# Kernel tuning notes

Hardware: AMD Instinct MI355X
Metric: run time of the kernel (lower is better)

Reference implementation:

```python
import jax, jax.numpy as jnp
import numpy as np

N_SAMPLES = 2048
BURN_IN = 128
STEP_SIZE = 0.1
D = 512   # walker dimension
H = 1024  # wavefunction MLP hidden width


def setup_inputs() -> dict:
    key = jax.random.key(0)
    k0, k1, k2 = jax.random.split(key, 3)
    x0 = jax.random.normal(k0, (1, D), dtype=jnp.float32)
    W1 = jax.random.normal(k1, (D, H), dtype=jnp.float32) / np.float32(np.sqrt(D))
    b1 = jnp.zeros((H,), dtype=jnp.float32)
    W2 = jax.random.normal(k2, (H, 1), dtype=jnp.float32) / np.float32(np.sqrt(H))
    b2 = jnp.zeros((1,), dtype=jnp.float32)
    return {"x0": x0, "W1": W1, "b1": b1, "W2": W2, "b2": b2}


def _model(x, W1, b1, W2, b2):
    # wavefunction MLP: [1, D] -> [1, 1]
    return jnp.tanh(x @ W1 + b1) @ W2 + b2


def reference(x0, W1, b1, W2, b2):
    def psi2(x):
        # model(x).pow(2)[0] -> shape [1]
        return (_model(x, W1, b1, W2, b2) ** 2)[0]

    def mh_step(x, k):
        k_noise, k_unif = jax.random.split(k)
        x_new = x + jax.random.normal(k_noise, x.shape, dtype=x.dtype) * STEP_SIZE
        p_new = psi2(x_new)
        p_old = psi2(x)
        ratio = jnp.minimum(p_new / (p_old + 1e-12), 1.0)          # clamp(max=1.0)
        u = jax.random.uniform(k_unif, ratio.shape, dtype=x.dtype)
        accept = (u < ratio).astype(x.dtype)[:, None]               # [1, 1]
        x = accept * x_new + (1.0 - accept) * x
        return x, x[0]  # carry chain state, record sample row [D]

    keys = jax.random.split(jax.random.key(1), N_SAMPLES + BURN_IN)
    _, traj = jax.lax.scan(mh_step, x0, keys)   # traj: [N+BURN_IN, D]
    return traj[BURN_IN:]                        # [N_SAMPLES, D]
```

## Files before the change

kernel.cpp:

```cpp
#include <hip/hip_runtime.h>
#include <stdint.h>
#include <math.h>


#define T_TOTAL 2176
#define NITER   1088
#define NROWS   2177
#define NBURN   128
#define DDIM    512
#define HDIM    1024
#define DONE_FLAG 0x13572468u

__device__ __forceinline__ uint2 tf2x32(uint32_t k0, uint32_t k1,
                                        uint32_t x0, uint32_t x1) {
  uint32_t ks2 = k0 ^ k1 ^ 0x1BD11BDAu;
  x0 += k0; x1 += k1;
#define TF_R(r) { x0 += x1; x1 = (x1 << (r)) | (x1 >> (32 - (r))); x1 ^= x0; }
  TF_R(13) TF_R(15) TF_R(26) TF_R(6)
  x0 += k1;  x1 += ks2 + 1u;
  TF_R(17) TF_R(29) TF_R(16) TF_R(24)
  x0 += ks2; x1 += k0 + 2u;
  TF_R(13) TF_R(15) TF_R(26) TF_R(6)
  x0 += k0;  x1 += k1 + 3u;
  TF_R(17) TF_R(29) TF_R(16) TF_R(24)
  x0 += k1;  x1 += ks2 + 4u;
  TF_R(13) TF_R(15) TF_R(26) TF_R(6)
  x0 += ks2; x1 += k0 + 5u;
#undef TF_R
  return make_uint2(x0, x1);
}

__device__ __forceinline__ float erfinv_xla(float x) {
  float w = -log1pf(-x * x);
  float p;
  if (w < 5.0f) {
    w = w - 2.5f;
    p = 2.81022636e-08f;
    p = fmaf(p, w, 3.43273939e-07f);
    p = fmaf(p, w, -3.5233877e-06f);
    p = fmaf(p, w, -4.39150654e-06f);
    p = fmaf(p, w, 0.00021858087f);
    p = fmaf(p, w, -0.00125372503f);
    p = fmaf(p, w, -0.00417768164f);
    p = fmaf(p, w, 0.246640727f);
    p = fmaf(p, w, 1.50140941f);
  } else {
    w = sqrtf(w) - 3.0f;
    p = -0.000200214257f;
    p = fmaf(p, w, 0.000100950558f);
    p = fmaf(p, w, 0.00134934322f);
    p = fmaf(p, w, -0.00367342844f);
    p = fmaf(p, w, 0.00573950773f);
    p = fmaf(p, w, -0.0076224613f);
    p = fmaf(p, w, 0.00943887047f);
    p = fmaf(p, w, 1.00167406f);
    p = fmaf(p, w, 2.83297682f);
  }
  return p * x;
}

__device__ __forceinline__ float normal_from_bits(uint32_t bits) {
  const float lo = -0.99999994f;
  float u01 = __uint_as_float(0x3f800000u | (bits >> 9)) - 1.0f;
  float v = u01 * 2.0f + lo;
  v = fmaxf(lo, v);
  return 1.41421356237309515f * erfinv_xla(v);
}

__device__ __forceinline__ float tanh_fast(float x) {
  float a = x * 2.88539008177792681472f;
#if __has_builtin(__builtin_amdgcn_exp2f)
  float e = __builtin_amdgcn_exp2f(a);
#else
  float e = exp2f(a);
#endif
  float r = __builtin_amdgcn_rcpf(e + 1.0f);
  return fmaf(-2.0f, r, 1.0f);
}

__global__ void __launch_bounds__(256) rng_kernel(const float* __restrict__ x0,
                                                  float* __restrict__ A,
                                                  float* __restrict__ U) {
  const uint32_t t = blockIdx.x;
  const int tid = threadIdx.x;
  uint2 kt = tf2x32(0u, 1u, 0u, t);
  uint2 kn = tf2x32(kt.x, kt.y, 0u, 0u);
  uint2 e0 = tf2x32(kn.x, kn.y, 0u, (uint32_t)tid);
  uint2 e1 = tf2x32(kn.x, kn.y, 0u, (uint32_t)(tid + 256));
  float n0 = normal_from_bits(e0.x ^ e0.y);
  float n1 = normal_from_bits(e1.x ^ e1.y);
  float* Arow = A + (size_t)(t + 1) * DDIM;
  Arow[tid]       = n0 * 0.1f;
  Arow[tid + 256] = n1 * 0.1f;
  if (tid == 0) {
    uint2 ku = tf2x32(kt.x, kt.y, 0u, 1u);
    uint2 eu = tf2x32(ku.x, ku.y, 0u, 0u);
    U[t] = __uint_as_float(0x3f800000u | ((eu.x ^ eu.y) >> 9)) - 1.0f;
  }
  if (t == 0) {
    A[tid]       = x0[tid];
    A[tid + 256] = x0[tid + 256];
  }
}

__global__ void __launch_bounds__(512) gemm_kernel(const float* __restrict__ A,
                                                   const float* __restrict__ W1,
                                                   float* __restrict__ Z,
                                                   int nrows) {
  const int r0 = blockIdx.x * 8;
  const int t  = threadIdx.x;
  const int c0 = t, c1 = t + 512;
  double acc[8][2];
#pragma unroll
  for (int r = 0; r < 8; ++r) { acc[r][0] = 0.0; acc[r][1] = 0.0; }
  for (int d = 0; d < 512; d += 4) {
    double wA[4], wB[4];
#pragma unroll
    for (int j = 0; j < 4; ++j) {
      wA[j] = (double)W1[(size_t)(d + j) * 1024 + c0];
      wB[j] = (double)W1[(size_t)(d + j) * 1024 + c1];
    }
#pragma unroll
    for (int r = 0; r < 8; ++r) {
      int rr = r0 + r; if (rr >= nrows) rr = nrows - 1;
      const float4 a4 = *(const float4*)(A + (size_t)rr * 512 + d);
      double a0 = (double)a4.x, a1 = (double)a4.y;
      double a2 = (double)a4.z, a3 = (double)a4.w;
      acc[r][0] += (a0 * wA[0] + a1 * wA[1]) + (a2 * wA[2] + a3 * wA[3]);
      acc[r][1] += (a0 * wB[0] + a1 * wB[1]) + (a2 * wB[2] + a3 * wB[3]);
    }
  }
  const int rmax = (nrows - r0 < 8) ? (nrows - r0) : 8;
  for (int r = 0; r < rmax; ++r) {
    Z[(size_t)(r0 + r) * 1024 + c0] = (float)acc[r][0];
    Z[(size_t)(r0 + r) * 1024 + c1] = (float)acc[r][1];
  }
}

#define DPP_ADD(v, ctrl)                                                     \
  v += __int_as_float(__builtin_amdgcn_update_dpp(                           \
      0, __float_as_int(v), (ctrl), 0xF, 0xF, true))

__device__ __forceinline__ float wave_reduce_to_last(float v) {
  DPP_ADD(v, 0xB1);
  DPP_ADD(v, 0x4E);
  DPP_ADD(v, 0x141);
  DPP_ADD(v, 0x140);
  DPP_ADD(v, 0x142);
  DPP_ADD(v, 0x143);
  return v;
}

#define BAR() asm volatile("s_waitcnt lgkmcnt(0)\n\ts_barrier" ::: "memory")

__global__ void __launch_bounds__(256) chain_kernel(
    const float* __restrict__ Z, const float* __restrict__ A,
    const float* __restrict__ U, const float* __restrict__ x0,
    const float* __restrict__ b1, const float* __restrict__ W2,
    const float* __restrict__ b2, float* __restrict__ out,
    unsigned* __restrict__ flag) {
  const int tid = threadIdx.x;

  if (blockIdx.x != 0) {
    float acc = (float)tid * 1.0e-6f;
    for (int i = 0; i < 4000; ++i) {
#pragma unroll
      for (int jj = 0; jj < 256; ++jj) acc = fmaf(acc, 0.99999988f, 1.0e-7f);
      unsigned f = __hip_atomic_load(flag, __ATOMIC_RELAXED,
                                     __HIP_MEMORY_SCOPE_AGENT);
      if (f == DONE_FLAG) break;
    }
    if (acc == 123456.75f && tid == 1023) out[0] = acc;
    return;
  }

  const int lane = tid & 63;
  const int wid = tid >> 6;
  __shared__ __align__(16) float wsum[2][3][4];
  __shared__ float Uld[2184];

  const float4* Zv = (const float4*)Z;
  const float2* Av = (const float2*)A;

  for (int i = tid; i < 2184; i += 256) Uld[i] = U[i];

  const float4 w2v = ((const float4*)W2)[tid];
  const float4 b1v = ((const float4*)b1)[tid];
  const float b2v = b2[0];

  float4 z0r = Zv[tid];
  float4 z1r = Zv[256 + tid];
  float4 z2r = Zv[512 + tid];
  float4 zA0 = Zv[3 * 256 + tid], zB0 = Zv[4 * 256 + tid];
  float4 zA1 = Zv[5 * 256 + tid], zB1 = Zv[6 * 256 + tid];
  float2 dAa0 = Av[1 * 256 + tid], dAb0 = Av[2 * 256 + tid];
  float2 dAa1 = Av[3 * 256 + tid], dAb1 = Av[4 * 256 + tid];

  double Y0 = (double)z0r.x + (double)b1v.x;
  double Y1 = (double)z0r.y + (double)b1v.y;
  double Y2 = (double)z0r.z + (double)b1v.z;
  double Y3 = (double)z0r.w + (double)b1v.w;

  float xa = x0[2 * tid], xb = x0[2 * tid + 1];

  __syncthreads();

  {
    float g0 = tanh_fast((float)Y0);
    float g1 = tanh_fast((float)Y1);
    float g2 = tanh_fast((float)Y2);
    float g3 = tanh_fast((float)Y3);
    float tm = fmaf(g3, w2v.w, fmaf(g2, w2v.z, fmaf(g1, w2v.y, g0 * w2v.x)));
    tm = wave_reduce_to_last(tm);
    if (lane == 63) wsum[1][0][wid] = tm;
  }
  __syncthreads();
  float p;
  {
    const float4 pp = *(const float4*)wsum[1][0];
    float m0 = ((pp.x + pp.y) + (pp.z + pp.w)) + b2v;
    p = m0 * m0;
  }
  float um1 = Uld[0] * (p + 1e-12f);
  float u2c = Uld[1];

  double Ya0 = Y0 + (double)z1r.x, Ya1 = Y1 + (double)z1r.y;
  double Ya2 = Y2 + (double)z1r.z, Ya3 = Y3 + (double)z1r.w;
  double Yb0 = Y0 + (double)z2r.x, Yb1 = Y1 + (double)z2r.y;
  double Yb2 = Y2 + (double)z2r.z, Yb3 = Y3 + (double)z2r.w;
  double Yc0 = Ya0 + (double)z2r.x, Yc1 = Ya1 + (double)z2r.y;
  double Yc2 = Ya2 + (double)z2r.z, Yc3 = Ya3 + (double)z2r.w;
  {
    float a0 = tanh_fast((float)Ya0), a1 = tanh_fast((float)Ya1);
    float a2 = tanh_fast((float)Ya2), a3 = tanh_fast((float)Ya3);
    float b0 = tanh_fast((float)Yb0), b1_ = tanh_fast((float)Yb1);
    float b2_ = tanh_fast((float)Yb2), b3 = tanh_fast((float)Yb3);
    float c0 = tanh_fast((float)Yc0), c1 = tanh_fast((float)Yc1);
    float c2 = tanh_fast((float)Yc2), c3 = tanh_fast((float)Yc3);
    float tA = fmaf(a3, w2v.w, fmaf(a2, w2v.z, fmaf(a1, w2v.y, a0 * w2v.x)));
    float tB = fmaf(b3, w2v.w, fmaf(b2_, w2v.z, fmaf(b1_, w2v.y, b0 * w2v.x)));
    float tC = fmaf(c3, w2v.w, fmaf(c2, w2v.z, fmaf(c1, w2v.y, c0 * w2v.x)));
    tA = wave_reduce_to_last(tA);
    tB = wave_reduce_to_last(tB);
    tC = wave_reduce_to_last(tC);
    if (lane == 63) {
      wsum[0][0][wid] = tA;
      wsum[0][1][wid] = tB;
      wsum[0][2][wid] = tC;
    }
  }
  __syncthreads();

#define ITER(k, PAR, ZAB, ZBB, DAB, DBB)                                     \
  {                                                                          \
    float u1n = Uld[2 * (k) + 2];                                            \
    float u2n = Uld[2 * (k) + 3];                                            \
    const float4 e1 = *(const float4*)wsum[PAR][0];                          \
    const float4 e2 = *(const float4*)wsum[PAR][1];                          \
    const float4 e3 = *(const float4*)wsum[PAR][2];                          \
    float m1 = ((e1.x + e1.y) + (e1.z + e1.w)) + b2v;                        \
    float q1 = m1 * m1;                                                      \
    bool a1v = um1 < q1;                                                     \
    float p1 = a1v ? q1 : p;                                                 \
    float um2 = u2c * (p1 + 1e-12f);                                         \
    float m2v = ((e2.x + e2.y) + (e2.z + e2.w)) + b2v;                       \
    float m3v = ((e3.x + e3.y) + (e3.z + e3.w)) + b2v;                       \
    float m23 = a1v ? m3v : m2v;                                             \
    float q23 = m23 * m23;                                                   \
    bool a2v = um2 < q23;                                                    \
    p = a2v ? q23 : p1;                                                      \
    float xat = a1v ? xa + DAB.x : xa;                                       \
    float xbt = a1v ? xb + DAB.y : xb;                                       \
    xa = a2v ? xat + DBB.x : xat;                                            \
    xb = a2v ? xbt + DBB.y : xbt;                                            \
    if ((k) >= 64) {                                                         \
      float2 o1; o1.x = xat; o1.y = xbt;                                     \
      *(float2*)(out + (size_t)(2 * (k) - NBURN) * DDIM + 2 * tid) = o1;     \
      float2 o2; o2.x = xa; o2.y = xb;                                       \
      *(float2*)(out + (size_t)(2 * (k) + 1 - NBURN) * DDIM + 2 * tid) = o2; \
    }                                                                        \
    DAB = Av[(size_t)(2 * (k) + 5) * 256 + tid];                             \
    DBB = Av[(size_t)(2 * (k) + 6) * 256 + tid];                             \
            \
    Y0 = a1v ? (a2v ? Yc0 : Ya0) : (a2v ? Yb0 : Y0);                         \
    Y1 = a1v ? (a2v ? Yc1 : Ya1) : (a2v ? Yb1 : Y1);                         \
    Y2 = a1v ? (a2v ? Yc2 : Ya2) : (a2v ? Yb2 : Y2);                         \
    Y3 = a1v ? (a2v ? Yc3 : Ya3) : (a2v ? Yb3 : Y3);                         \
                         \
    Ya0 = Y0 + (double)ZAB.x;  Ya1 = Y1 + (double)ZAB.y;                     \
    Ya2 = Y2 + (double)ZAB.z;  Ya3 = Y3 + (double)ZAB.w;                     \
    Yb0 = Y0 + (double)ZBB.x;  Yb1 = Y1 + (double)ZBB.y;                     \
    Yb2 = Y2 + (double)ZBB.z;  Yb3 = Y3 + (double)ZBB.w;                     \
    Yc0 = Ya0 + (double)ZBB.x; Yc1 = Ya1 + (double)ZBB.y;                    \
    Yc2 = Ya2 + (double)ZBB.z; Yc3 = Ya3 + (double)ZBB.w;                    \
    ZAB = Zv[(size_t)(2 * (k) + 7) * 256 + tid];                             \
    ZBB = Zv[(size_t)(2 * (k) + 8) * 256 + tid];                             \
    float ga0 = tanh_fast((float)Ya0), ga1 = tanh_fast((float)Ya1);          \
    float ga2 = tanh_fast((float)Ya2), ga3 = tanh_fast((float)Ya3);          \
    float gb0 = tanh_fast((float)Yb0), gb1 = tanh_fast((float)Yb1);          \
    float gb2 = tanh_fast((float)Yb2), gb3 = tanh_fast((float)Yb3);          \
    float gc0 = tanh_fast((float)Yc0), gc1 = tanh_fast((float)Yc1);          \
    float gc2 = tanh_fast((float)Yc2), gc3 = tanh_fast((float)Yc3);          \
    float tA = fmaf(ga3, w2v.w, fmaf(ga2, w2v.z, fmaf(ga1, w2v.y, ga0 * w2v.x))); \
    float tB = fmaf(gb3, w2v.w, fmaf(gb2, w2v.z, fmaf(gb1, w2v.y, gb0 * w2v.x))); \
    float tC = fmaf(gc3, w2v.w, fmaf(gc2, w2v.z, fmaf(gc1, w2v.y, gc0 * w2v.x))); \
    tA = wave_reduce_to_last(tA);                                            \
    tB = wave_reduce_to_last(tB);                                            \
    tC = wave_reduce_to_last(tC);                                            \
    if (lane == 63) {                                                        \
      wsum[(PAR) ^ 1][0][wid] = tA;                                          \
      wsum[(PAR) ^ 1][1][wid] = tB;                                          \
      wsum[(PAR) ^ 1][2][wid] = tC;                                          \
    }                                                                        \
    um1 = u1n * (p + 1e-12f);                                                \
    u2c = u2n;                                                               \
    BAR();                                                                   \
  }

  for (int k = 0; k < NITER; k += 2) {
    ITER(k,     0, zA0, zB0, dAa0, dAb0);
    ITER(k + 1, 1, zA1, zB1, dAa1, dAb1);
  }
#undef ITER

  if (tid == 0) {
    __hip_atomic_store(flag, DONE_FLAG, __ATOMIC_RELAXED,
                       __HIP_MEMORY_SCOPE_AGENT);
  }
}

extern "C" void kernel_launch(void* const* d_in, const int* in_sizes, int n_in,
                              void* d_out, int out_size, void* d_ws, size_t ws_size,
                              hipStream_t stream) {
  const float* x0 = (const float*)d_in[0];
  const float* W1 = (const float*)d_in[1];
  const float* b1 = (const float*)d_in[2];
  const float* W2 = (const float*)d_in[3];
  const float* b2 = (const float*)d_in[4];
  float* out = (float*)d_out;

  char* ws = (char*)d_ws;
  float* A = (float*)ws;
  float* Z = (float*)(ws + 4472832);
  float* U = (float*)(ws + 4472832 + 8945664);
  unsigned* flag = (unsigned*)(ws + 4472832 + 8945664 + 8736);

  rng_kernel<<<T_TOTAL, 256, 0, stream>>>(x0, A, U);
  gemm_kernel<<<273, 512, 0, stream>>>(A, W1, Z, NROWS);
  chain_kernel<<<256, 256, 0, stream>>>(Z, A, U, x0, b1, W2, b2, out, flag);
}
```

Before: 861.8 us.

## Widen chain kernel to 512 threads and double GEMM rows per block

```diff
diff --git a/kernel.cpp b/kernel.cpp
--- a/kernel.cpp
+++ b/kernel.cpp
@@ -107,12 +107,12 @@
                                                    const float* __restrict__ W1,
                                                    float* __restrict__ Z,
                                                    int nrows) {
-  const int r0 = blockIdx.x * 8;
+  const int r0 = blockIdx.x * 16;
   const int t  = threadIdx.x;
   const int c0 = t, c1 = t + 512;
-  double acc[8][2];
+  double acc[16][2];
 #pragma unroll
-  for (int r = 0; r < 8; ++r) { acc[r][0] = 0.0; acc[r][1] = 0.0; }
+  for (int r = 0; r < 16; ++r) { acc[r][0] = 0.0; acc[r][1] = 0.0; }
   for (int d = 0; d < 512; d += 4) {
     double wA[4], wB[4];
 #pragma unroll
@@ -121,7 +121,7 @@
       wB[j] = (double)W1[(size_t)(d + j) * 1024 + c1];
     }
 #pragma unroll
-    for (int r = 0; r < 8; ++r) {
+    for (int r = 0; r < 16; ++r) {
       int rr = r0 + r; if (rr >= nrows) rr = nrows - 1;
       const float4 a4 = *(const float4*)(A + (size_t)rr * 512 + d);
       double a0 = (double)a4.x, a1 = (double)a4.y;
@@ -130,7 +130,7 @@
       acc[r][1] += (a0 * wB[0] + a1 * wB[1]) + (a2 * wB[2] + a3 * wB[3]);
     }
   }
-  const int rmax = (nrows - r0 < 8) ? (nrows - r0) : 8;
+  const int rmax = (nrows - r0 < 16) ? (nrows - r0) : 16;
   for (int r = 0; r < rmax; ++r) {
     Z[(size_t)(r0 + r) * 1024 + c0] = (float)acc[r][0];
     Z[(size_t)(r0 + r) * 1024 + c1] = (float)acc[r][1];
@@ -153,7 +153,7 @@
 
 #define BAR() asm volatile("s_waitcnt lgkmcnt(0)\n\ts_barrier" ::: "memory")
 
-__global__ void __launch_bounds__(256) chain_kernel(
+__global__ void __launch_bounds__(512) chain_kernel(
     const float* __restrict__ Z, const float* __restrict__ A,
     const float* __restrict__ U, const float* __restrict__ x0,
     const float* __restrict__ b1, const float* __restrict__ W2,
@@ -176,70 +176,61 @@
 
   const int lane = tid & 63;
   const int wid = tid >> 6;
-  __shared__ __align__(16) float wsum[2][3][4];
+  __shared__ __align__(16) float wsum[2][3][8];
   __shared__ float Uld[2184];
 
-  const float4* Zv = (const float4*)Z;
-  const float2* Av = (const float2*)A;
-
-  for (int i = tid; i < 2184; i += 256) Uld[i] = U[i];
-
-  const float4 w2v = ((const float4*)W2)[tid];
-  const float4 b1v = ((const float4*)b1)[tid];
+  const float2* Zv = (const float2*)Z;
+
+  for (int i = tid; i < 2184; i += 512) Uld[i] = U[i];
+
+  const float2 w2v = ((const float2*)W2)[tid];
+  const float2 b1v = ((const float2*)b1)[tid];
   const float b2v = b2[0];
 
-  float4 z0r = Zv[tid];
-  float4 z1r = Zv[256 + tid];
-  float4 z2r = Zv[512 + tid];
-  float4 zA0 = Zv[3 * 256 + tid], zB0 = Zv[4 * 256 + tid];
-  float4 zA1 = Zv[5 * 256 + tid], zB1 = Zv[6 * 256 + tid];
-  float2 dAa0 = Av[1 * 256 + tid], dAb0 = Av[2 * 256 + tid];
-  float2 dAa1 = Av[3 * 256 + tid], dAb1 = Av[4 * 256 + tid];
+  float2 z0r = Zv[tid];
+  float2 z1r = Zv[512 + tid];
+  float2 z2r = Zv[1024 + tid];
+  float2 zA0 = Zv[3 * 512 + tid], zB0 = Zv[4 * 512 + tid];
+  float2 zA1 = Zv[5 * 512 + tid], zB1 = Zv[6 * 512 + tid];
+  float dAa0 = A[1 * 512 + tid], dAb0 = A[2 * 512 + tid];
+  float dAa1 = A[3 * 512 + tid], dAb1 = A[4 * 512 + tid];
 
   double Y0 = (double)z0r.x + (double)b1v.x;
   double Y1 = (double)z0r.y + (double)b1v.y;
-  double Y2 = (double)z0r.z + (double)b1v.z;
-  double Y3 = (double)z0r.w + (double)b1v.w;
-
-  float xa = x0[2 * tid], xb = x0[2 * tid + 1];
+
+  float xa = x0[tid];
 
   __syncthreads();
 
   {
     float g0 = tanh_fast((float)Y0);
     float g1 = tanh_fast((float)Y1);
-    float g2 = tanh_fast((float)Y2);
-    float g3 = tanh_fast((float)Y3);
-    float tm = fmaf(g3, w2v.w, fmaf(g2, w2v.z, fmaf(g1, w2v.y, g0 * w2v.x)));
+    float tm = fmaf(g1, w2v.y, g0 * w2v.x);
     tm = wave_reduce_to_last(tm);
     if (lane == 63) wsum[1][0][wid] = tm;
   }
   __syncthreads();
   float p;
   {
-    const float4 pp = *(const float4*)wsum[1][0];
-    float m0 = ((pp.x + pp.y) + (pp.z + pp.w)) + b2v;
+    const float4 qa = *(const float4*)&wsum[1][0][0];
+    const float4 qb = *(const float4*)&wsum[1][0][4];
+    float m0 = (((qa.x + qa.y) + (qa.z + qa.w)) +
+                ((qb.x + qb.y) + (qb.z + qb.w))) + b2v;
     p = m0 * m0;
   }
   float um1 = Uld[0] * (p + 1e-12f);
   float u2c = Uld[1];
 
   double Ya0 = Y0 + (double)z1r.x, Ya1 = Y1 + (double)z1r.y;
-  double Ya2 = Y2 + (double)z1r.z, Ya3 = Y3 + (double)z1r.w;
   double Yb0 = Y0 + (double)z2r.x, Yb1 = Y1 + (double)z2r.y;
-  double Yb2 = Y2 + (double)z2r.z, Yb3 = Y3 + (double)z2r.w;
   double Yc0 = Ya0 + (double)z2r.x, Yc1 = Ya1 + (double)z2r.y;
-  double Yc2 = Ya2 + (double)z2r.z, Yc3 = Ya3 + (double)z2r.w;
   {
     float a0 = tanh_fast((float)Ya0), a1 = tanh_fast((float)Ya1);
-    float a2 = tanh_fast((float)Ya2), a3 = tanh_fast((float)Ya3);
     float b0 = tanh_fast((float)Yb0), b1_ = tanh_fast((float)Yb1);
-    float b2_ = tanh_fast((float)Yb2), b3 = tanh_fast((float)Yb3);
     float c0 = tanh_fast((float)Yc0), c1 = tanh_fast((float)Yc1);
-    float c2 = tanh_fast((float)Yc2), c3 = tanh_fast((float)Yc3);
-    float tA = fmaf(a3, w2v.w, fmaf(a2, w2v.z, fmaf(a1, w2v.y, a0 * w2v.x)));
-    float tB = fmaf(b3, w2v.w, fmaf(b2_, w2v.z, fmaf(b1_, w2v.y, b0 * w2v.x)));
-    float tC = fmaf(c3, w2v.w, fmaf(c2, w2v.z, fmaf(c1, w2v.y, c0 * w2v.x)));
+    float tA = fmaf(a1, w2v.y, a0 * w2v.x);
+    float tB = fmaf(b1_, w2v.y, b0 * w2v.x);
+    float tC = fmaf(c1, w2v.y, c0 * w2v.x);
     tA = wave_reduce_to_last(tA);
     tB = wave_reduce_to_last(tB);
     tC = wave_reduce_to_last(tC);
@@ -255,55 +246,47 @@
   {                                                                          \
     float u1n = Uld[2 * (k) + 2];                                            \
     float u2n = Uld[2 * (k) + 3];                                            \
-    const float4 e1 = *(const float4*)wsum[PAR][0];                          \
-    const float4 e2 = *(const float4*)wsum[PAR][1];                          \
-    const float4 e3 = *(const float4*)wsum[PAR][2];                          \
-    float m1 = ((e1.x + e1.y) + (e1.z + e1.w)) + b2v;                        \
+    const float4 e1a = *(const float4*)&wsum[PAR][0][0];                     \
+    const float4 e1b = *(const float4*)&wsum[PAR][0][4];                     \
+    const float4 e2a = *(const float4*)&wsum[PAR][1][0];                     \
+    const float4 e2b = *(const float4*)&wsum[PAR][1][4];                     \
+    const float4 e3a = *(const float4*)&wsum[PAR][2][0];                     \
+    const float4 e3b = *(const float4*)&wsum[PAR][2][4];                     \
+    float m1 = (((e1a.x + e1a.y) + (e1a.z + e1a.w)) +                        \
+                ((e1b.x + e1b.y) + (e1b.z + e1b.w))) + b2v;                  \
     float q1 = m1 * m1;                                                      \
     bool a1v = um1 < q1;                                                     \
     float p1 = a1v ? q1 : p;                                                 \
     float um2 = u2c * (p1 + 1e-12f);                                         \
-    float m2v = ((e2.x + e2.y) + (e2.z + e2.w)) + b2v;                       \
-    float m3v = ((e3.x + e3.y) + (e3.z + e3.w)) + b2v;                       \
+    float m2v = (((e2a.x + e2a.y) + (e2a.z + e2a.w)) +                       \
+                 ((e2b.x + e2b.y) + (e2b.z + e2b.w))) + b2v;                 \
+    float m3v = (((e3a.x + e3a.y) + (e3a.z + e3a.w)) +                       \
+                 ((e3b.x + e3b.y) + (e3b.z + e3b.w))) + b2v;                 \
     float m23 = a1v ? m3v : m2v;                                             \
     float q23 = m23 * m23;                                                   \
     bool a2v = um2 < q23;                                                    \
     p = a2v ? q23 : p1;                                                      \
-    float xat = a1v ? xa + DAB.x : xa;                                       \
-    float xbt = a1v ? xb + DAB.y : xb;                                       \
-    xa = a2v ? xat + DBB.x : xat;                                            \
-    xb = a2v ? xbt + DBB.y : xbt;                                            \
+    float xat = a1v ? xa + DAB : xa;                                         \
+    xa = a2v ? xat + DBB : xat;                                              \
     if ((k) >= 64) {                                                         \
-      float2 o1; o1.x = xat; o1.y = xbt;                                     \
-      *(float2*)(out + (size_t)(2 * (k) - NBURN) * DDIM + 2 * tid) = o1;     \
-      float2 o2; o2.x = xa; o2.y = xb;                                       \
-      *(float2*)(out + (size_t)(2 * (k) + 1 - NBURN) * DDIM + 2 * tid) = o2; \
+      out[(size_t)(2 * (k) - NBURN) * DDIM + tid] = xat;                     \
+      out[(size_t)(2 * (k) + 1 - NBURN) * DDIM + tid] = xa;                  \
     }                                                                        \
-    DAB = Av[(size_t)(2 * (k) + 5) * 256 + tid];                             \
-    DBB = Av[(size_t)(2 * (k) + 6) * 256 + tid];                             \
-            \
+    DAB = A[(size_t)(2 * (k) + 5) * 512 + tid];                              \
+    DBB = A[(size_t)(2 * (k) + 6) * 512 + tid];                              \
     Y0 = a1v ? (a2v ? Yc0 : Ya0) : (a2v ? Yb0 : Y0);                         \
     Y1 = a1v ? (a2v ? Yc1 : Ya1) : (a2v ? Yb1 : Y1);                         \
-    Y2 = a1v ? (a2v ? Yc2 : Ya2) : (a2v ? Yb2 : Y2);                         \
-    Y3 = a1v ? (a2v ? Yc3 : Ya3) : (a2v ? Yb3 : Y3);                         \
-                         \
     Ya0 = Y0 + (double)ZAB.x;  Ya1 = Y1 + (double)ZAB.y;                     \
-    Ya2 = Y2 + (double)ZAB.z;  Ya3 = Y3 + (double)ZAB.w;                     \
     Yb0 = Y0 + (double)ZBB.x;  Yb1 = Y1 + (double)ZBB.y;                     \
-    Yb2 = Y2 + (double)ZBB.z;  Yb3 = Y3 + (double)ZBB.w;                     \
     Yc0 = Ya0 + (double)ZBB.x; Yc1 = Ya1 + (double)ZBB.y;                    \
-    Yc2 = Ya2 + (double)ZBB.z; Yc3 = Ya3 + (double)ZBB.w;                    \
-    ZAB = Zv[(size_t)(2 * (k) + 7) * 256 + tid];                             \
-    ZBB = Zv[(size_t)(2 * (k) + 8) * 256 + tid];                             \
+    ZAB = Zv[(size_t)(2 * (k) + 7) * 512 + tid];                             \
+    ZBB = Zv[(size_t)(2 * (k) + 8) * 512 + tid];                             \
     float ga0 = tanh_fast((float)Ya0), ga1 = tanh_fast((float)Ya1);          \
-    float ga2 = tanh_fast((float)Ya2), ga3 = tanh_fast((float)Ya3);          \
     float gb0 = tanh_fast((float)Yb0), gb1 = tanh_fast((float)Yb1);          \
-    float gb2 = tanh_fast((float)Yb2), gb3 = tanh_fast((float)Yb3);          \
     float gc0 = tanh_fast((float)Yc0), gc1 = tanh_fast((float)Yc1);          \
-    float gc2 = tanh_fast((float)Yc2), gc3 = tanh_fast((float)Yc3);          \
-    float tA = fmaf(ga3, w2v.w, fmaf(ga2, w2v.z, fmaf(ga1, w2v.y, ga0 * w2v.x))); \
-    float tB = fmaf(gb3, w2v.w, fmaf(gb2, w2v.z, fmaf(gb1, w2v.y, gb0 * w2v.x))); \
-    float tC = fmaf(gc3, w2v.w, fmaf(gc2, w2v.z, fmaf(gc1, w2v.y, gc0 * w2v.x))); \
+    float tA = fmaf(ga1, w2v.y, ga0 * w2v.x);                                \
+    float tB = fmaf(gb1, w2v.y, gb0 * w2v.x);                                \
+    float tC = fmaf(gc1, w2v.y, gc0 * w2v.x);                                \
     tA = wave_reduce_to_last(tA);                                            \
     tB = wave_reduce_to_last(tB);                                            \
     tC = wave_reduce_to_last(tC);                                            \
@@ -346,6 +329,6 @@
   unsigned* flag = (unsigned*)(ws + 4472832 + 8945664 + 8736);
 
   rng_kernel<<<T_TOTAL, 256, 0, stream>>>(x0, A, U);
-  gemm_kernel<<<273, 512, 0, stream>>>(A, W1, Z, NROWS);
-  chain_kernel<<<256, 256, 0, stream>>>(Z, A, U, x0, b1, W2, b2, out, flag);
-}
+  gemm_kernel<<<137, 512, 0, stream>>>(A, W1, Z, NROWS);
+  chain_kernel<<<256, 512, 0, stream>>>(Z, A, U, x0, b1, W2, b2, out, flag);
+}
```

Result: slower. 919.9 us (+6.7%).
